# Performance work log

Hardware: AMD Instinct MI355X
Metric: run time of the kernel (lower is better)

Reference implementation:

```python
import jax, jax.numpy as jnp
import numpy as np

ALPHA = 0.2  # leaky_relu negative slope
NEG_INF = -9e15


def _gat_stage(x, adj_mask, W, a):
    """Multi-head dense GAT layer (concat=True).
    x: [N, Fin], adj_mask: [N, N] bool, W: [H, Fin, O], a: [H, 2*O].
    Returns [N, H*O].
    """
    O = W.shape[-1]
    Wh = jnp.einsum('nf,hfo->hno', x, W)                 # [H, N, O]
    f1 = jnp.einsum('hno,ho->hn', Wh, a[:, :O])          # a_src . Wh_i
    f2 = jnp.einsum('hno,ho->hn', Wh, a[:, O:])          # a_dst . Wh_j
    e = f1[:, :, None] + f2[:, None, :]                  # [H, N, N]
    e = jnp.where(e > 0, e, ALPHA * e)                   # leaky_relu
    e = jnp.where(adj_mask[None], e, NEG_INF)            # mask non-edges
    att = jax.nn.softmax(e, axis=-1)                     # row softmax over neighbors
    h = jnp.einsum('hnm,hmo->hno', att, Wh)              # aggregate
    h = jax.nn.elu(h)                                    # concat=True -> elu
    H, N, _ = h.shape
    return jnp.transpose(h, (1, 0, 2)).reshape(N, H * O)  # head concat


def setup_inputs() -> dict:
    key = jax.random.key(0)
    ks = jax.random.split(key, 12)
    N, F0, NHID, H, NCLASS = 4096, 512, 64, 4, 40
    x = jax.random.normal(ks[0], (N, F0), jnp.float32)
    adj = jax.random.randint(ks[1], (N, N), 0, 2, jnp.int32)
    s = 0.05
    W1 = jax.random.normal(ks[2], (H, F0, NHID), jnp.float32) * s
    a1 = jax.random.normal(ks[3], (H, 2 * NHID), jnp.float32) * s
    W2 = jax.random.normal(ks[4], (4, H * NHID, 32), jnp.float32) * s
    a2 = jax.random.normal(ks[5], (4, 64), jnp.float32) * s
    W3 = jax.random.normal(ks[6], (4, 4 * 32, 16), jnp.float32) * s
    a3 = jax.random.normal(ks[7], (4, 32), jnp.float32) * s
    Wlin = jax.random.normal(ks[8], (4 * 16, NCLASS), jnp.float32) * s
    blin = jnp.zeros((NCLASS,), jnp.float32)
    return {"x": x, "adj": adj, "W1": W1, "a1": a1, "W2": W2, "a2": a2,
            "W3": W3, "a3": a3, "Wlin": Wlin, "blin": blin}


def reference(x, adj, W1, a1, W2, a2, W3, a3, Wlin, blin):
    # eval mode: all F.dropout calls are identity
    m = adj > 0
    h = _gat_stage(x, m, W1, a1)    # [N, 256]
    h = _gat_stage(h, m, W2, a2)    # [N, 128]
    h = _gat_stage(h, m, W3, a3)    # [N, 64]
    logits = h @ Wlin + blin        # [N, nclass]
    return jax.nn.log_softmax(logits, axis=1)
```

## Files before the change

kernel.cpp:

```cpp
#include <hip/hip_runtime.h>
#include <hip/hip_bf16.h>
#include <stdint.h>

typedef __attribute__((ext_vector_type(8))) short short8;
typedef __attribute__((ext_vector_type(4))) float float4v;

#define NHEADS 4
#define NNODES 4096
#define LOG2E 1.4426950408889634f
#define PSTR ((size_t)NHEADS * NNODES * 64)
#define LSTR ((size_t)NHEADS * NNODES)

__device__ __forceinline__ unsigned short f2b(float x) {
    union { float f; uint32_t u; } v; v.f = x;
    uint32_t u = v.u;
    uint32_t r = (u + 0x7FFFu + ((u >> 16) & 1u)) >> 16;
    return (unsigned short)r;
}
__device__ __forceinline__ float b2f(unsigned short s) {
    union { uint32_t u; float f; } v; v.u = ((uint32_t)s) << 16;
    return v.f;
}
__device__ __forceinline__ uint32_t cvtpk(float lo, float hi) {
    uint32_t r;
    asm("v_cvt_pk_bf16_f32 %0, %1, %2" : "=v"(r) : "v"(lo), "v"(hi));
    return r;
}

#define AS1 __attribute__((address_space(1)))
#define AS3 __attribute__((address_space(3)))
__device__ __forceinline__ void gl_lds16(const void* g, void* l) {
    __builtin_amdgcn_global_load_lds((const AS1 unsigned int*)g,
                                     (AS3 unsigned int*)l, 16, 0, 0);
}

__global__ __launch_bounds__(256) void k_pack(const int* __restrict__ adj,
                                              unsigned long long* __restrict__ mask) {
    int w = (blockIdx.x * 256 + threadIdx.x) >> 6;
    int lane = threadIdx.x & 63;
    int row = w >> 6;
    int chunk = w & 63;
    int j = chunk * 64 + lane;
    int v = adj[(size_t)row * NNODES + j];
    unsigned long long b = __ballot(v != 0);
    if (lane == 0) mask[row * 64 + chunk] = b;
}

__global__ __launch_bounds__(256) void k_convert(const float* __restrict__ x,
                                                 unsigned short* __restrict__ xbf,
                                                 const float* __restrict__ W1,
                                                 unsigned short* __restrict__ WT1,
                                                 const float* __restrict__ W2,
                                                 unsigned short* __restrict__ WT2,
                                                 const float* __restrict__ W3,
                                                 unsigned short* __restrict__ WT3) {
    int i = blockIdx.x * 256 + threadIdx.x;
    if (i < 524288) {
        float4v v = ((const float4v*)x)[i];
        uint2 r;
        r.x = cvtpk(v[0], v[1]);
        r.y = cvtpk(v[2], v[3]);
        ((uint2*)xbf)[i] = r;
    } else if (i < 524288 + 131072) {
        int j = i - 524288;
        int o = j & 63, f = (j >> 6) & 511, h = j >> 15;
        WT1[((size_t)(h * 64 + o)) * 512 + f] = f2b(W1[j]);
    } else if (i < 524288 + 131072 + 32768) {
        int j = i - 655360;
        int o = j & 31, f = (j >> 5) & 255, h = j >> 13;
        WT2[((size_t)(h * 32 + o)) * 256 + f] = f2b(W2[j]);
    } else {
        int j = i - 688128;
        int o = j & 15, f = (j >> 4) & 127, h = j >> 11;
        WT3[((size_t)(h * 16 + o)) * 128 + f] = f2b(W3[j]);
    }
}

template <int Fin, int O>
__global__ __launch_bounds__(256) void k_whgemm(const unsigned short* __restrict__ A,
                                                const unsigned short* __restrict__ WT,
                                                const float* __restrict__ avec,
                                                unsigned short* __restrict__ WhT,
                                                float* __restrict__ f1,
                                                float* __restrict__ f2) {
    __shared__ float scc[4][16][64];
    constexpr int HPB = 64 / O;
    const int rt = blockIdx.x & 255, cg = blockIdx.x >> 8;
    const int wv = threadIdx.x >> 6, lane = threadIdx.x & 63;
    const int il = lane & 15, g = lane >> 4;
    constexpr int kpw = Fin >> 2;
    const int k0 = wv * kpw;
    float4v acc[4];
#pragma unroll
    for (int ot = 0; ot < 4; ++ot) acc[ot] = (float4v){0.f, 0.f, 0.f, 0.f};
    const unsigned short* Arow = A + (size_t)(rt * 16 + il) * Fin + k0 + 8 * g;
    const unsigned short* Bcol = WT + (size_t)(cg * 64 + il) * Fin + k0 + 8 * g;
#pragma unroll
    for (int k = 0; k < kpw; k += 32) {
        short8 af = *(const short8*)(Arow + k);
#pragma unroll
        for (int ot = 0; ot < 4; ++ot) {
            short8 bf = *(const short8*)(Bcol + (size_t)ot * 16 * Fin + k);
            acc[ot] = __builtin_amdgcn_mfma_f32_16x16x32_bf16(af, bf, acc[ot], 0, 0, 0);
        }
    }
#pragma unroll
    for (int ot = 0; ot < 4; ++ot)
#pragma unroll
        for (int r = 0; r < 4; ++r) scc[wv][g * 4 + r][ot * 16 + il] = acc[ot][r];
    __syncthreads();
    for (int e = threadIdx.x; e < 1024; e += 256) {
        int row = e >> 6, col = e & 63;
        float v = scc[0][row][col] + scc[1][row][col] + scc[2][row][col] + scc[3][row][col];
        int gc = cg * 64 + col;
        int hh = gc / O, o = gc % O;
        WhT[((size_t)(hh * O + o)) * NNODES + rt * 16 + row] = f2b(v);
    }
    {
        int hl = lane / O, o = lane % O;
        int h = cg * HPB + hl;
        float av1 = avec[h * 2 * O + o];
        float av2 = avec[h * 2 * O + O + o];
#pragma unroll
        for (int r = 0; r < 4; ++r) {
            int row = wv * 4 + r;
            float v = scc[0][row][lane] + scc[1][row][lane] + scc[2][row][lane] + scc[3][row][lane];
            float s1 = v * av1, s2 = v * av2;
#pragma unroll
            for (int d = O / 2; d > 0; d >>= 1) {
                s1 += __shfl_xor(s1, d);
                s2 += __shfl_xor(s2, d);
            }
            if (o == 0) {
                int n = rt * 16 + row;
                f1[h * NNODES + n] = s1 * LOG2E;
                f2[h * NNODES + n] = s2 * LOG2E;
            }
        }
    }
}

template <int O>
__device__ __forceinline__ void stage_tile(const unsigned short* WB0, int j0,
                                           char* dst, int tid) {
    constexpr int CH = O * 8;
#pragma unroll
    for (int q = 0; q < CH; q += 256) {
        int s = q + tid;
        if (s < CH) {
            int o = s >> 3, c = s & 7;
            int cg = c ^ (o & 7);
            gl_lds16(WB0 + (size_t)o * NNODES + j0 + 8 * cg, dst + s * 16);
        }
    }
}

template <int O>
__global__ __launch_bounds__(256, 6) void k_pv(const uint32_t* __restrict__ mask,
                                               const float* __restrict__ f1L,
                                               const float* __restrict__ f2L,
                                               const unsigned short* __restrict__ WhT,
                                               float* __restrict__ pacc,
                                               float* __restrict__ lpart) {
    constexpr int NT = O / 16;
    constexpr int CH = O * 8;
    __shared__ unsigned short bt[2][CH * 8];
    __shared__ float sf2[1024];
    const int b = blockIdx.x;
    const int js = b & 3, rt = (b >> 2) & 63, h = b >> 8;
    const int tid = threadIdx.x, wv = tid >> 6, lane = tid & 63;
    const int il = lane & 15, g = lane >> 4;
    const int j0b = js * 1024;
    const float* f2h = f2L + h * NNODES;
    const unsigned short* WB0 = WhT + (size_t)h * O * NNODES;
    const int n = rt * 64 + wv * 16 + il;
    const float f1i = f1L[h * NNODES + n];
    const uint32_t* mr = mask + (size_t)n * 128 + js * 32;

    gl_lds16(f2h + j0b + tid * 4, (char*)sf2 + tid * 16);
    stage_tile<O>(WB0, j0b, (char*)&bt[0][0], tid);
    uint2 mw = *(const uint2*)mr;
    __syncthreads();

    float4v acc[NT];
#pragma unroll
    for (int ot = 0; ot < NT; ++ot) acc[ot] = (float4v){0.f, 0.f, 0.f, 0.f};
    float4v accl = (float4v){0.f, 0.f, 0.f, 0.f};
    short8 bones;
#pragma unroll
    for (int q = 0; q < 8; ++q) bones[q] = (il == 0) ? (short)0x3F80 : (short)0;

    int cur = 0;
    for (int t = 0; t < 16; ++t) {
        if (t < 15) stage_tile<O>(WB0, j0b + (t + 1) * 64, (char*)&bt[cur ^ 1][0], tid);
        uint2 mwn = mw;
        if (t < 15) mwn = *(const uint2*)(mr + (t + 1) * 2);
        const char* btc = (const char*)&bt[cur][0];
        const float* fp0 = sf2 + t * 64 + 8 * g;
#pragma unroll
        for (int s = 0; s < 2; ++s) {
            short8 B[NT];
#pragma unroll
            for (int ot = 0; ot < NT; ++ot) {
                int o = ot * 16 + il;
                B[ot] = *(const short8*)(btc + o * 128 + 16 * (((s << 2) + g) ^ (il & 7)));
            }
            const float* fp = fp0 + s * 32;
            float4v fa = *(const float4v*)fp;
            float4v fb = *(const float4v*)(fp + 4);
            uint32_t word = s ? mw.y : mw.x;
            uint32_t bits = (word >> (8 * g)) & 0xFFu;
            float p[8];
#pragma unroll
            for (int bb = 0; bb < 8; ++bb) {
                float sv = f1i + ((bb < 4) ? fa[bb] : fb[bb - 4]);
                sv = fmaxf(sv, 0.2f * sv);
                float pv = __builtin_amdgcn_exp2f(sv);
                p[bb] = ((bits >> bb) & 1u) ? pv : 0.f;
            }
            union { short8 s8; uint32_t u[4]; } pu;
            pu.u[0] = cvtpk(p[0], p[1]);
            pu.u[1] = cvtpk(p[2], p[3]);
            pu.u[2] = cvtpk(p[4], p[5]);
            pu.u[3] = cvtpk(p[6], p[7]);
#pragma unroll
            for (int ot = 0; ot < NT; ++ot)
                acc[ot] = __builtin_amdgcn_mfma_f32_16x16x32_bf16(pu.s8, B[ot], acc[ot], 0, 0, 0);
            accl = __builtin_amdgcn_mfma_f32_16x16x32_bf16(pu.s8, bones, accl, 0, 0, 0);
        }
        __syncthreads();
        cur ^= 1;
        mw = mwn;
    }

    float* pj = pacc + js * PSTR + (size_t)h * NNODES * O;
#pragma unroll
    for (int ot = 0; ot < NT; ++ot)
#pragma unroll
        for (int r = 0; r < 4; ++r)
            pj[(size_t)(rt * 64 + wv * 16 + g * 4 + r) * O + ot * 16 + il] = acc[ot][r];
    if (il == 0) {
        float* lj = lpart + js * LSTR + h * NNODES;
#pragma unroll
        for (int r = 0; r < 4; ++r)
            lj[rt * 64 + wv * 16 + g * 4 + r] = accl[r];
    }
}

template <int O>
__global__ __launch_bounds__(256) void k_fin(const float* __restrict__ pacc,
                                             const float* __restrict__ lpart,
                                             unsigned short* __restrict__ hout) {
    constexpr int HO = NHEADS * O;
    int e = blockIdx.x * 256 + threadIdx.x;
    int o = e % O;
    int n = (e / O) & (NNODES - 1);
    int h = e / (O * NNODES);
    size_t idx = ((size_t)h * NNODES + n) * O + o;
    float s = pacc[idx] + pacc[PSTR + idx] + pacc[2 * PSTR + idx] + pacc[3 * PSTR + idx];
    int li = h * NNODES + n;
    float l = lpart[li] + lpart[LSTR + li] + lpart[2 * LSTR + li] + lpart[3 * LSTR + li];
    float v = s / l;
    v = (v > 0.f) ? v : (__expf(v) - 1.f);
    hout[(size_t)n * HO + h * O + o] = f2b(v);
}

__global__ __launch_bounds__(256) void k_final(const unsigned short* __restrict__ h3,
                                               const float* __restrict__ Wlin,
                                               const float* __restrict__ blin,
                                               float* __restrict__ out) {
    int n = blockIdx.x * 4 + (threadIdx.x >> 6);
    int lane = threadIdx.x & 63;
    float logit = 0.f;
    if (lane < 40) {
        logit = blin[lane];
        for (int k = 0; k < 64; ++k) {
            logit += b2f(h3[n * 64 + k]) * Wlin[k * 40 + lane];
        }
    }
    float mv = (lane < 40) ? logit : -3.0e38f;
    for (int d = 32; d > 0; d >>= 1) mv = fmaxf(mv, __shfl_xor(mv, d));
    float ex = (lane < 40) ? __expf(logit - mv) : 0.f;
    for (int d = 32; d > 0; d >>= 1) ex += __shfl_xor(ex, d);
    if (lane < 40) out[n * 40 + lane] = logit - mv - logf(ex);
}

template <int Fin, int O>
static void run_stage(hipStream_t stream, const uint32_t* mask, const unsigned short* xin,
                      const unsigned short* WT, const float* avec,
                      unsigned short* WhT, float* f1, float* f2,
                      float* pacc, float* lpart, unsigned short* hout) {
    constexpr int CG = (NHEADS * O) / 64;
    k_whgemm<Fin, O><<<256 * CG, 256, 0, stream>>>(xin, WT, avec, WhT, f1, f2);
    k_pv<O><<<1024, 256, 0, stream>>>(mask, f1, f2, WhT, pacc, lpart);
    k_fin<O><<<NHEADS * NNODES * O / 256, 256, 0, stream>>>(pacc, lpart, hout);
}

extern "C" void kernel_launch(void* const* d_in, const int* in_sizes, int n_in,
                              void* d_out, int out_size, void* d_ws, size_t ws_size,
                              hipStream_t stream) {
    const float* x    = (const float*)d_in[0];
    const int*   adj  = (const int*)d_in[1];
    const float* W1   = (const float*)d_in[2];
    const float* a1   = (const float*)d_in[3];
    const float* W2   = (const float*)d_in[4];
    const float* a2   = (const float*)d_in[5];
    const float* W3   = (const float*)d_in[6];
    const float* a3   = (const float*)d_in[7];
    const float* Wlin = (const float*)d_in[8];
    const float* blin = (const float*)d_in[9];
    float* out = (float*)d_out;

    char* ws = (char*)d_ws;
    uint32_t*       mask = (uint32_t*)ws;
    unsigned short* xbf  = (unsigned short*)(ws + (2u << 20));
    unsigned short* WhT  = (unsigned short*)(ws + (6u << 20));
    unsigned short* WT1  = (unsigned short*)(ws + (8u << 20));
    unsigned short* WT2  = (unsigned short*)(ws + (8u << 20) + (256u << 10));
    unsigned short* WT3  = (unsigned short*)(ws + (8u << 20) + (320u << 10));
    float*          f1   = (float*)(ws + (8u << 20) + (384u << 10));
    float*          f2   = (float*)(ws + (8u << 20) + (448u << 10));
    float*          lpart= (float*)(ws + (8u << 20) + (512u << 10));
    float*          pacc = (float*)(ws + (9u << 20));

    k_pack<<<65536, 256, 0, stream>>>(adj, (unsigned long long*)mask);
    k_convert<<<2720, 256, 0, stream>>>(x, xbf, W1, WT1, W2, WT2, W3, WT3);

    run_stage<512, 64>(stream, mask, xbf, WT1, a1, WhT, f1, f2, pacc, lpart, xbf);
    run_stage<256, 32>(stream, mask, xbf, WT2, a2, WhT, f1, f2, pacc, lpart, xbf);
    run_stage<128, 16>(stream, mask, xbf, WT3, a3, WhT, f1, f2, pacc, lpart, xbf);

    k_final<<<NNODES / 4, 256, 0, stream>>>(xbf, Wlin, blin, out);
}
```

Measured before the change: 158.3 us.

## Triple-buffer PV tiles with one barrier per step, stage mask in LDS, merge prep kernels

```diff
diff --git a/kernel.cpp b/kernel.cpp
--- a/kernel.cpp
+++ b/kernel.cpp
@@ -34,27 +34,29 @@
                                      (AS3 unsigned int*)l, 16, 0, 0);
 }
 
-__global__ __launch_bounds__(256) void k_pack(const int* __restrict__ adj,
-                                              unsigned long long* __restrict__ mask) {
-    int w = (blockIdx.x * 256 + threadIdx.x) >> 6;
-    int lane = threadIdx.x & 63;
-    int row = w >> 6;
-    int chunk = w & 63;
-    int j = chunk * 64 + lane;
-    int v = adj[(size_t)row * NNODES + j];
-    unsigned long long b = __ballot(v != 0);
-    if (lane == 0) mask[row * 64 + chunk] = b;
-}
-
-__global__ __launch_bounds__(256) void k_convert(const float* __restrict__ x,
-                                                 unsigned short* __restrict__ xbf,
-                                                 const float* __restrict__ W1,
-                                                 unsigned short* __restrict__ WT1,
-                                                 const float* __restrict__ W2,
-                                                 unsigned short* __restrict__ WT2,
-                                                 const float* __restrict__ W3,
-                                                 unsigned short* __restrict__ WT3) {
-    int i = blockIdx.x * 256 + threadIdx.x;
+__global__ __launch_bounds__(256) void k_pre(const int* __restrict__ adj,
+                                             unsigned long long* __restrict__ mask,
+                                             const float* __restrict__ x,
+                                             unsigned short* __restrict__ xbf,
+                                             const float* __restrict__ W1,
+                                             unsigned short* __restrict__ WT1,
+                                             const float* __restrict__ W2,
+                                             unsigned short* __restrict__ WT2,
+                                             const float* __restrict__ W3,
+                                             unsigned short* __restrict__ WT3) {
+    int b = blockIdx.x;
+    if (b < 65536) {
+        int w = (b * 256 + threadIdx.x) >> 6;
+        int lane = threadIdx.x & 63;
+        int row = w >> 6;
+        int chunk = w & 63;
+        int j = chunk * 64 + lane;
+        int v = adj[(size_t)row * NNODES + j];
+        unsigned long long bm = __ballot(v != 0);
+        if (lane == 0) mask[row * 64 + chunk] = bm;
+        return;
+    }
+    int i = (b - 65536) * 256 + threadIdx.x;
     if (i < 524288) {
         float4v v = ((const float4v*)x)[i];
         uint2 r;
@@ -69,7 +71,7 @@
         int j = i - 655360;
         int o = j & 31, f = (j >> 5) & 255, h = j >> 13;
         WT2[((size_t)(h * 32 + o)) * 256 + f] = f2b(W2[j]);
-    } else {
+    } else if (i < 524288 + 131072 + 32768 + 8192) {
         int j = i - 688128;
         int o = j & 15, f = (j >> 4) & 127, h = j >> 11;
         WT3[((size_t)(h * 16 + o)) * 128 + f] = f2b(W3[j]);
@@ -147,7 +149,7 @@
 #pragma unroll
     for (int q = 0; q < CH; q += 256) {
         int s = q + tid;
-        if (s < CH) {
+        if (CH >= 256 || s < CH) {
             int o = s >> 3, c = s & 7;
             int cg = c ^ (o & 7);
             gl_lds16(WB0 + (size_t)o * NNODES + j0 + 8 * cg, dst + s * 16);
@@ -156,7 +158,7 @@
 }
 
 template <int O>
-__global__ __launch_bounds__(256, 6) void k_pv(const uint32_t* __restrict__ mask,
+__global__ __launch_bounds__(256, 4) void k_pv(const uint32_t* __restrict__ mask,
                                                const float* __restrict__ f1L,
                                                const float* __restrict__ f2L,
                                                const unsigned short* __restrict__ WhT,
@@ -164,8 +166,10 @@
                                                float* __restrict__ lpart) {
     constexpr int NT = O / 16;
     constexpr int CH = O * 8;
-    __shared__ unsigned short bt[2][CH * 8];
+    constexpr int LPT = (O == 64) ? 2 : 1;
+    __shared__ unsigned short bt[3][CH * 8];
     __shared__ float sf2[1024];
+    __shared__ uint32_t smask[64][34];
     const int b = blockIdx.x;
     const int js = b & 3, rt = (b >> 2) & 63, h = b >> 8;
     const int tid = threadIdx.x, wv = tid >> 6, lane = tid & 63;
@@ -173,14 +177,27 @@
     const int j0b = js * 1024;
     const float* f2h = f2L + h * NNODES;
     const unsigned short* WB0 = WhT + (size_t)h * O * NNODES;
-    const int n = rt * 64 + wv * 16 + il;
-    const float f1i = f1L[h * NNODES + n];
-    const uint32_t* mr = mask + (size_t)n * 128 + js * 32;
-
+    const int nrow = wv * 16 + il;
+    const float f1i = f1L[h * NNODES + rt * 64 + nrow];
+
+    {
+        int r = tid >> 2, c = (tid & 3) * 8;
+        const uint32_t* mg = mask + (size_t)(rt * 64 + r) * 128 + js * 32 + c;
+        uint4 m0 = *(const uint4*)mg;
+        uint4 m1 = *(const uint4*)(mg + 4);
+        asm volatile("s_waitcnt vmcnt(0)" ::: "memory");
+        uint32_t* dstm = &smask[r][c];
+        *(uint2*)(dstm + 0) = make_uint2(m0.x, m0.y);
+        *(uint2*)(dstm + 2) = make_uint2(m0.z, m0.w);
+        *(uint2*)(dstm + 4) = make_uint2(m1.x, m1.y);
+        *(uint2*)(dstm + 6) = make_uint2(m1.z, m1.w);
+    }
     gl_lds16(f2h + j0b + tid * 4, (char*)sf2 + tid * 16);
     stage_tile<O>(WB0, j0b, (char*)&bt[0][0], tid);
-    uint2 mw = *(const uint2*)mr;
-    __syncthreads();
+    stage_tile<O>(WB0, j0b + 64, (char*)&bt[1][0], tid);
+    asm volatile("s_waitcnt vmcnt(%0) lgkmcnt(0)" :: "i"(LPT) : "memory");
+    __builtin_amdgcn_sched_barrier(0);
+    __builtin_amdgcn_s_barrier();
 
     float4v acc[NT];
 #pragma unroll
@@ -190,12 +207,8 @@
 #pragma unroll
     for (int q = 0; q < 8; ++q) bones[q] = (il == 0) ? (short)0x3F80 : (short)0;
 
-    int cur = 0;
-    for (int t = 0; t < 16; ++t) {
-        if (t < 15) stage_tile<O>(WB0, j0b + (t + 1) * 64, (char*)&bt[cur ^ 1][0], tid);
-        uint2 mwn = mw;
-        if (t < 15) mwn = *(const uint2*)(mr + (t + 1) * 2);
-        const char* btc = (const char*)&bt[cur][0];
+    auto compute = [&](int t, const char* btc) {
+        uint2 mw = *(const uint2*)&smask[nrow][2 * t];
         const float* fp0 = sf2 + t * 64 + 8 * g;
 #pragma unroll
         for (int s = 0; s < 2; ++s) {
@@ -228,10 +241,20 @@
                 acc[ot] = __builtin_amdgcn_mfma_f32_16x16x32_bf16(pu.s8, B[ot], acc[ot], 0, 0, 0);
             accl = __builtin_amdgcn_mfma_f32_16x16x32_bf16(pu.s8, bones, accl, 0, 0, 0);
         }
-        __syncthreads();
-        cur ^= 1;
-        mw = mwn;
-    }
+    };
+
+    for (int t = 0; t < 14; ++t) {
+        stage_tile<O>(WB0, j0b + (t + 2) * 64, (char*)&bt[(t + 2) % 3][0], tid);
+        compute(t, (const char*)&bt[t % 3][0]);
+        asm volatile("s_waitcnt vmcnt(%0)" :: "i"(LPT) : "memory");
+        __builtin_amdgcn_sched_barrier(0);
+        __builtin_amdgcn_s_barrier();
+    }
+    compute(14, (const char*)&bt[2][0]);
+    asm volatile("s_waitcnt vmcnt(0)" ::: "memory");
+    __builtin_amdgcn_sched_barrier(0);
+    __builtin_amdgcn_s_barrier();
+    compute(15, (const char*)&bt[0][0]);
 
     float* pj = pacc + js * PSTR + (size_t)h * NNODES * O;
 #pragma unroll
@@ -323,8 +346,8 @@
     float*          lpart= (float*)(ws + (8u << 20) + (512u << 10));
     float*          pacc = (float*)(ws + (9u << 20));
 
-    k_pack<<<65536, 256, 0, stream>>>(adj, (unsigned long long*)mask);
-    k_convert<<<2720, 256, 0, stream>>>(x, xbf, W1, WT1, W2, WT2, W3, WT3);
+    k_pre<<<65536 + 2720, 256, 0, stream>>>(adj, (unsigned long long*)mask, x, xbf,
+                                            W1, WT1, W2, WT2, W3, WT3);
 
     run_stage<512, 64>(stream, mask, xbf, WT1, a1, WhT, f1, f2, pacc, lpart, xbf);
     run_stage<256, 32>(stream, mask, xbf, WT2, a2, WhT, f1, f2, pacc, lpart, xbf);
```

Measured after the change: 150.9 us. 1.05x faster.
